# Kernel tuning notes

Hardware: AMD Instinct MI355X
Metric: run time of the kernel (lower is better)

Reference implementation:

```python
import jax, jax.numpy as jnp
import numpy as np

D_MODEL = 1024
N_HEADS = 16
D_K = D_MODEL // N_HEADS


def setup_inputs() -> dict:
    key = jax.random.key(0)
    ks = jax.random.split(key, 16)
    B, S = 2, 2048
    sc = 1.0 / np.sqrt(D_MODEL)
    inp = {
        "query": jax.random.normal(ks[0], (B, S, D_MODEL), jnp.float32),
        "key": jax.random.normal(ks[1], (B, S, D_MODEL), jnp.float32),
        "value": jax.random.normal(ks[2], (B, S, D_MODEL), jnp.float32),
        "Wq": jax.random.normal(ks[3], (D_MODEL, D_MODEL), jnp.float32) * sc,
        "bq": jnp.zeros((D_MODEL,), jnp.float32),
        "Wk": jax.random.normal(ks[4], (D_MODEL, D_MODEL), jnp.float32) * sc,
        "bk": jnp.zeros((D_MODEL,), jnp.float32),
        "Wv": jax.random.normal(ks[5], (D_MODEL, D_MODEL), jnp.float32) * sc,
        "bv": jnp.zeros((D_MODEL,), jnp.float32),
        "Wo": jax.random.normal(ks[6], (D_MODEL, D_MODEL), jnp.float32) * sc,
        "bo": jnp.zeros((D_MODEL,), jnp.float32),
        "theta": jax.random.normal(ks[7], (N_HEADS,), jnp.float32) * 0.1,
        "gate": jax.random.normal(ks[8], (D_MODEL,), jnp.float32) * 0.1,
    }
    return inp


def reference(query, key, value, Wq, bq, Wk, bk, Wv, bv, Wo, bo, theta, gate):
    B, Sq, D = query.shape
    Sk = key.shape[1]
    # linear projections (torch Linear: x @ W.T + b), split heads -> [B,H,S,d_k]
    Q = (query @ Wq.T + bq).reshape(B, Sq, N_HEADS, D_K).transpose(0, 2, 1, 3)
    K = (key @ Wk.T + bk).reshape(B, Sk, N_HEADS, D_K).transpose(0, 2, 1, 3)
    V = (value @ Wv.T + bv).reshape(B, Sk, N_HEADS, D_K).transpose(0, 2, 1, 3)

    inv_sqrt_dk = 1.0 / jnp.sqrt(jnp.float32(D_K))
    scores = jnp.einsum("bhqd,bhkd->bhqk", Q, K) * inv_sqrt_dk

    # per-head rotation of the first two feature dims of Q
    cos_t = jnp.cos(theta)[None, :, None, None]  # [1,H,1,1]
    sin_t = jnp.sin(theta)[None, :, None, None]
    q_rot = jnp.concatenate(
        [
            cos_t * Q[..., :1] - sin_t * Q[..., 1:2],
            sin_t * Q[..., :1] + cos_t * Q[..., 1:2],
            Q[..., 2:],
        ],
        axis=-1,
    )
    scores_q = jnp.einsum("bhqd,bhkd->bhqk", q_rot, K) * inv_sqrt_dk

    g_scalar = jax.nn.sigmoid(gate.mean())
    scores = g_scalar * scores_q + (1.0 - g_scalar) * scores

    attn = jax.nn.softmax(scores, axis=-1)
    out = jnp.einsum("bhqk,bhkd->bhqd", attn, V)
    out = out.transpose(0, 2, 1, 3).reshape(B, Sq, D)
    return out @ Wo.T + bo
```

## Files before the change

### kernel.cpp

```cpp
#include <hip/hip_runtime.h>


typedef __bf16 bf16;
typedef __attribute__((ext_vector_type(8))) bf16 bf16x8;
typedef __attribute__((ext_vector_type(4))) bf16 bf16x4;
typedef __attribute__((ext_vector_type(2))) bf16 bf16x2;
typedef __attribute__((ext_vector_type(4))) float f32x4;
typedef __attribute__((ext_vector_type(4))) short s16x4;
typedef unsigned int u32;

#define D_MODEL 1024
#define NH 16
#define DKH 64
#define SEQ 2048

#define GLL16(g, l) __builtin_amdgcn_global_load_lds(                      \
    (const __attribute__((address_space(1))) void*)(g),                    \
    (__attribute__((address_space(3))) void*)(l), 16, 0, 0)

static __device__ __forceinline__ f32x4 mfma16(bf16x8 a, bf16x8 b, f32x4 c) {
  return __builtin_amdgcn_mfma_f32_16x16x32_bf16(a, b, c, 0, 0, 0);
}

#if __has_builtin(__builtin_amdgcn_mfma_f32_16x16x16bf16_1k)
#define HAVE_MFMA_K16 1
static __device__ __forceinline__ f32x4 mfma16k16(s16x4 a, s16x4 b, f32x4 c) {
  return __builtin_amdgcn_mfma_f32_16x16x16bf16_1k(a, b, c, 0, 0, 0);
}
#else
#define HAVE_MFMA_K16 0
#endif

static __device__ __forceinline__ u32 pk2(float a, float b) {
  bf16x2 v; v[0] = (bf16)a; v[1] = (bf16)b;
  return __builtin_bit_cast(u32, v);
}

static __device__ __forceinline__ float fexp2(float x) {
#if __has_builtin(__builtin_amdgcn_exp2f)
  return __builtin_amdgcn_exp2f(x);
#else
  return exp2f(x);
#endif
}

#define CQK 0.1803368801111244f

__global__ __launch_bounds__(256) void prep(const float* __restrict__ query,
                                            const float* __restrict__ key,
                                            const float* __restrict__ value,
                                            const float* __restrict__ Wq,
                                            const float* __restrict__ bq,
                                            const float* __restrict__ Wk,
                                            const float* __restrict__ Wv,
                                            const float* __restrict__ Wo,
                                            const float* __restrict__ gate,
                                            const float* __restrict__ theta,
                                            bf16* __restrict__ Xq,
                                            bf16* __restrict__ Xk,
                                            bf16* __restrict__ Xv,
                                            bf16* __restrict__ Wqp,
                                            bf16* __restrict__ Wkp,
                                            bf16* __restrict__ Wvp,
                                            bf16* __restrict__ Wop,
                                            float* __restrict__ bqp) {
  const int id = blockIdx.x;
  const int tid = threadIdx.x;
  if (id >= 4096) {
    const int rem = id - 4096;
    const int iz = rem >> 12;
    const int ib = rem & 4095;
    const float* s = (iz == 0) ? query : (iz == 1) ? key : value;
    bf16* d = (iz == 0) ? Xq : (iz == 1) ? Xk : Xv;
    const size_t i = (size_t)(ib * 256 + tid) * 4;
    float4 w = *(const float4*)(s + i);
    bf16x4 o; o[0] = (bf16)w.x; o[1] = (bf16)w.y; o[2] = (bf16)w.z; o[3] = (bf16)w.w;
    *(bf16x4*)(d + i) = o;
    return;
  }
  const int wz = id >> 10, wb = id & 1023;
  if (wz != 0) {
    const float* s = (wz == 1) ? Wk : (wz == 2) ? Wv : Wo;
    bf16* dd = (wz == 1) ? Wkp : (wz == 2) ? Wvp : Wop;
    const size_t i = (size_t)(wb * 256 + tid) * 4;
    float4 v = *(const float4*)(s + i);
    bf16x4 o4; o4[0] = (bf16)v.x; o4[1] = (bf16)v.y; o4[2] = (bf16)v.z; o4[3] = (bf16)v.w;
    *(bf16x4*)(dd + i) = o4;
    return;
  }
  __shared__ float red[4];
  float ssum = 0.f;
  for (int i = tid; i < D_MODEL; i += 256) ssum += gate[i];
#pragma unroll
  for (int off = 32; off > 0; off >>= 1) ssum += __shfl_down(ssum, off);
  if ((tid & 63) == 0) red[tid >> 6] = ssum;
  __syncthreads();
  const float g = 1.f / (1.f + __expf(-(red[0] + red[1] + red[2] + red[3]) / 1024.f));

  const int t = wb * 256 + tid;
  const int r = t >> 8;
  const int c0 = (t & 255) * 4;
  const int d = r & 63, h = r >> 6;
  float4 w = *(const float4*)(Wq + (size_t)r * D_MODEL + c0);
  float4 o;
  if (d == 0) {
    const float a = (g * cosf(theta[h]) + (1.f - g)) * CQK;
    const float bb = (g * sinf(theta[h])) * CQK;
    float4 w2 = *(const float4*)(Wq + (size_t)(r + 1) * D_MODEL + c0);
    o.x = a * w.x - bb * w2.x; o.y = a * w.y - bb * w2.y;
    o.z = a * w.z - bb * w2.z; o.w = a * w.w - bb * w2.w;
    if (c0 == 0) bqp[r] = a * bq[r] - bb * bq[r + 1];
  } else if (d == 1) {
    const float a = (g * cosf(theta[h]) + (1.f - g)) * CQK;
    const float bb = (g * sinf(theta[h])) * CQK;
    float4 w2 = *(const float4*)(Wq + (size_t)(r - 1) * D_MODEL + c0);
    o.x = bb * w2.x + a * w.x; o.y = bb * w2.y + a * w.y;
    o.z = bb * w2.z + a * w.z; o.w = bb * w2.w + a * w.w;
    if (c0 == 0) bqp[r] = bb * bq[r - 1] + a * bq[r];
  } else {
    o.x = CQK * w.x; o.y = CQK * w.y;
    o.z = CQK * w.z; o.w = CQK * w.w;
    if (c0 == 0) bqp[r] = CQK * bq[r];
  }
  bf16x4 ov; ov[0] = (bf16)o.x; ov[1] = (bf16)o.y; ov[2] = (bf16)o.z; ov[3] = (bf16)o.w;
  *(bf16x4*)(Wqp + (size_t)r * D_MODEL + c0) = ov;
}

static __device__ __forceinline__ void gemm_bt_main(const bf16* __restrict__ A,
                                                    const bf16* __restrict__ Bt,
                                                    int tm, int tn, int K,
                                                    f32x4 acc[4][4]) {
  __shared__ bf16 lA[8192];
  __shared__ bf16 lB[8192];
  const int tid = threadIdx.x;
  const int lane = tid & 63, wv = tid >> 6;
  const int wm = wv >> 1, wn = wv & 1;
  const int l16 = lane & 15, lg = lane >> 4;

#pragma unroll
  for (int i = 0; i < 4; ++i)
#pragma unroll
    for (int j = 0; j < 4; ++j) acc[i][j] = (f32x4){0.f, 0.f, 0.f, 0.f};

  int offA[4][2], offB[4][2];
#pragma unroll
  for (int f = 0; f < 4; ++f)
#pragma unroll
    for (int kc = 0; kc < 2; ++kc) {
      const int m = wm * 64 + f * 16 + l16;
      offA[f][kc] = m * 64 + (((kc * 4 + lg) ^ (m & 7)) << 3);
      const int n = wn * 64 + f * 16 + l16;
      offB[f][kc] = n * 64 + (((kc * 4 + lg) ^ (n & 7)) << 3);
    }

  const int rowb = tid >> 3, oct = tid & 7;
  const int soct = oct ^ (rowb & 7);
  const bf16* gA[4];
  const bf16* gB[4];
#pragma unroll
  for (int rd = 0; rd < 4; ++rd) {
    gA[rd] = A + (size_t)(tm + rd * 32 + rowb) * K + soct * 8;
    gB[rd] = Bt + (size_t)(tn + rd * 32 + rowb) * K + soct * 8;
  }

  for (int kt = 0; kt < K; kt += 64) {
    __syncthreads();
#pragma unroll
    for (int rd = 0; rd < 4; ++rd) {
      GLL16(gA[rd] + kt, &lA[rd * 2048 + wv * 512]);
      GLL16(gB[rd] + kt, &lB[rd * 2048 + wv * 512]);
    }
    __syncthreads();
#pragma unroll
    for (int kc = 0; kc < 2; ++kc) {
      bf16x8 af[4], bv[4];
#pragma unroll
      for (int f = 0; f < 4; ++f) {
        af[f] = *(const bf16x8*)&lA[offA[f][kc]];
        bv[f] = *(const bf16x8*)&lB[offB[f][kc]];
      }
#pragma unroll
      for (int i = 0; i < 4; ++i)
#pragma unroll
        for (int j = 0; j < 4; ++j)
          acc[i][j] = mfma16(af[i], bv[j], acc[i][j]);
    }
  }
}

__global__ __launch_bounds__(256) void gemm_qkv(
    const bf16* __restrict__ Xq, const bf16* __restrict__ Xk, const bf16* __restrict__ Xv,
    const bf16* __restrict__ Wq, const bf16* __restrict__ Wk, const bf16* __restrict__ Wv,
    const float* __restrict__ bqp, const float* __restrict__ bk, const float* __restrict__ bv,
    bf16* __restrict__ Qp, bf16* __restrict__ Kp, bf16* __restrict__ Vt) {
  const int wgp = (blockIdx.x & 7) * 96 + (blockIdx.x >> 3);
  const int z = wgp >> 8;
  const int rem = wgp & 255;
  const int tm = (rem >> 3) * 128, tn = (rem & 7) * 128;
  const bf16* A = (z == 0) ? Xq : (z == 1) ? Xk : Xv;
  const bf16* Bt = (z == 0) ? Wq : (z == 1) ? Wk : Wv;
  const float* bias = (z == 0) ? bqp : (z == 1) ? bk : bv;
  f32x4 acc[4][4];
  gemm_bt_main(A, Bt, tm, tn, D_MODEL, acc);
  const int lane = threadIdx.x & 63, wv = threadIdx.x >> 6;
  const int wm = wv >> 1, wn = wv & 1, l16 = lane & 15, lg = lane >> 4;
  if (z < 2) {
    bf16* C = (z == 0) ? Qp : Kp;
#pragma unroll
    for (int i = 0; i < 4; ++i) {
      const int m0 = tm + wm * 64 + i * 16 + lg * 4;
#pragma unroll
      for (int j = 0; j < 4; ++j) {
        const int n = tn + wn * 64 + j * 16 + l16;
        const float bb = bias[n];
        const int h = n >> 6, d = n & 63;
#pragma unroll
        for (int r = 0; r < 4; ++r) {
          const int m = m0 + r;
          const int b = m >> 11, s = m & 2047;
          C[((size_t)(b * NH + h) * SEQ + s) * DKH + d] = (bf16)(acc[i][j][r] + bb);
        }
      }
    }
  } else {
#pragma unroll
    for (int i = 0; i < 4; ++i) {
      const int m0 = tm + wm * 64 + i * 16 + lg * 4;
      const int b = m0 >> 11, s0 = m0 & 2047;
#pragma unroll
      for (int j = 0; j < 4; ++j) {
        const int n = tn + wn * 64 + j * 16 + l16;
        const float bb = bias[n];
        const int h = n >> 6, d = n & 63;
        bf16x4 ov;
#pragma unroll
        for (int r = 0; r < 4; ++r) ov[r] = (bf16)(acc[i][j][r] + bb);
        *(bf16x4*)&Vt[((size_t)(b * NH + h) * DKH + d) * SEQ + s0] = ov;
      }
    }
  }
}

__global__ __launch_bounds__(256) void gemm_out_k(const bf16* __restrict__ A,
                                                  const bf16* __restrict__ Bt,
                                                  const float* __restrict__ bias,
                                                  float* __restrict__ C) {
  const int wgp = (blockIdx.x & 7) * 32 + (blockIdx.x >> 3);
  const int tm = (wgp >> 3) * 128, tn = (wgp & 7) * 128;
  f32x4 acc[4][4];
  gemm_bt_main(A, Bt, tm, tn, D_MODEL, acc);
  const int lane = threadIdx.x & 63, wv = threadIdx.x >> 6;
  const int wm = wv >> 1, wn = wv & 1, l16 = lane & 15, lg = lane >> 4;
#pragma unroll
  for (int i = 0; i < 4; ++i) {
    const int m0 = tm + wm * 64 + i * 16 + lg * 4;
#pragma unroll
    for (int j = 0; j < 4; ++j) {
      const int n = tn + wn * 64 + j * 16 + l16;
      const float bb = bias[n];
#pragma unroll
      for (int r = 0; r < 4; ++r)
        C[(size_t)(m0 + r) * D_MODEL + n] = acc[i][j][r] + bb;
    }
  }
}

__global__ __launch_bounds__(256, 4) void attn_kernel(const bf16* __restrict__ Qp,
                                                      const bf16* __restrict__ Kp,
                                                      const bf16* __restrict__ Vt,
                                                      bf16* __restrict__ Op) {
  __shared__ bf16 lK[4096];
  __shared__ bf16 lV[4096];
#if !HAVE_MFMA_K16
  __shared__ bf16 lP[4096];
#endif

  const int tid = threadIdx.x;
  const int lane = tid & 63, w = tid >> 6;
  const int l16 = lane & 15, lg = lane >> 4;
  const int wgp = (blockIdx.x & 7) * 128 + (blockIdx.x >> 3);
  const int bh = wgp >> 5;
  const int b = bh >> 4, h = bh & 15;
  const int q0 = (wgp & 31) * 64;
  const size_t kvb = (size_t)bh * SEQ * DKH;

  bf16x8 aq[2];
#pragma unroll
  for (int kc = 0; kc < 2; ++kc)
    aq[kc] = *(const bf16x8*)&Qp[kvb + (size_t)(q0 + w * 16 + l16) * DKH + kc * 32 + lg * 8];

  f32x4 o[4];
#pragma unroll
  for (int fn = 0; fn < 4; ++fn) o[fn] = (f32x4){0.f, 0.f, 0.f, 0.f};
  float m_run = -1e30f, l_run = 0.f;

  const int kr = tid >> 3, oct = tid & 7;
  const bf16* gK = Kp + kvb + (size_t)kr * DKH + oct * 8;
  const bf16* gV = Vt + kvb + (size_t)kr * SEQ + oct * 8;
  const int swz0 = kr * 64 + ((oct ^ (kr & 7)) << 3);
  const int swz1 = (kr + 32) * 64 + ((oct ^ (kr & 7)) << 3);

#if !HAVE_MFMA_K16
  bf16* lPw = &lP[w * 1024];
  int pwr[4];
#pragma unroll
  for (int fn = 0; fn < 4; ++fn)
    pwr[fn] = l16 * 64 + (((fn * 2 + (lg >> 1)) ^ (l16 & 7)) << 3) + ((lg & 1) << 2);
  int prd[2];
#pragma unroll
  for (int kc = 0; kc < 2; ++kc)
    prd[kc] = l16 * 64 + (((kc * 4 + lg) ^ (l16 & 7)) << 3);
#endif

  bf16x8 k0r = *(const bf16x8*)(gK);
  bf16x8 k1r = *(const bf16x8*)(gK + 32 * DKH);
  bf16x8 v0r = *(const bf16x8*)(gV);
  bf16x8 v1r = *(const bf16x8*)(gV + (size_t)32 * SEQ);

  for (int kt = 0; kt < SEQ; kt += 64) {
    __syncthreads();
    *(bf16x8*)&lK[swz0] = k0r;  *(bf16x8*)&lK[swz1] = k1r;
    *(bf16x8*)&lV[swz0] = v0r;  *(bf16x8*)&lV[swz1] = v1r;
    __syncthreads();
    if (kt + 64 < SEQ) {
      k0r = *(const bf16x8*)(gK + (size_t)(kt + 64) * DKH);
      k1r = *(const bf16x8*)(gK + (size_t)(kt + 96) * DKH);
      v0r = *(const bf16x8*)(gV + (kt + 64));
      v1r = *(const bf16x8*)(gV + (size_t)32 * SEQ + (kt + 64));
    }

    f32x4 st[4];
    __builtin_amdgcn_s_setprio(1);
#pragma unroll
    for (int fn = 0; fn < 4; ++fn) {
      const int row = fn * 16 + l16;
      bf16x8 ka = *(const bf16x8*)&lK[row * 64 + ((lg ^ (row & 7)) << 3)];
      bf16x8 kb = *(const bf16x8*)&lK[row * 64 + (((4 + lg) ^ (row & 7)) << 3)];
      f32x4 t = (f32x4){0.f, 0.f, 0.f, 0.f};
      t = mfma16(ka, aq[0], t);
      t = mfma16(kb, aq[1], t);
      st[fn] = t;
    }
    __builtin_amdgcn_s_setprio(0);

    float pm = fmaxf(fmaxf(fmaxf(st[0][0], st[0][1]), fmaxf(st[0][2], st[0][3])),
                     fmaxf(fmaxf(st[1][0], st[1][1]), fmaxf(st[1][2], st[1][3])));
    pm = fmaxf(pm, fmaxf(fmaxf(fmaxf(st[2][0], st[2][1]), fmaxf(st[2][2], st[2][3])),
                         fmaxf(fmaxf(st[3][0], st[3][1]), fmaxf(st[3][2], st[3][3]))));
    pm = fmaxf(pm, __shfl_xor(pm, 16));
    pm = fmaxf(pm, __shfl_xor(pm, 32));

    if (!__all(pm <= m_run + 8.f)) {
      const float mnew = fmaxf(m_run, pm);
      const float alpha = fexp2(m_run - mnew);
      m_run = mnew;
      l_run *= alpha;
      float a4[4];
#pragma unroll
      for (int r = 0; r < 4; ++r) a4[r] = __shfl(alpha, (lg << 4) | (lg * 4 + r));
#pragma unroll
      for (int fn = 0; fn < 4; ++fn)
#pragma unroll
        for (int r = 0; r < 4; ++r) o[fn][r] *= a4[r];
    }

    float rs = 0.f;
#if HAVE_MFMA_K16
    s16x4 paf[4];
#endif
#pragma unroll
    for (int fn = 0; fn < 4; ++fn) {
      const float p0 = fexp2(st[fn][0] - m_run);
      const float p1 = fexp2(st[fn][1] - m_run);
      const float p2 = fexp2(st[fn][2] - m_run);
      const float p3 = fexp2(st[fn][3] - m_run);
      rs += (p0 + p1) + (p2 + p3);
      uint2 pw; pw.x = pk2(p0, p1); pw.y = pk2(p2, p3);
#if HAVE_MFMA_K16
      paf[fn] = __builtin_bit_cast(s16x4, pw);
#else
      *(uint2*)&lPw[pwr[fn]] = pw;
#endif
    }
    rs += __shfl_xor(rs, 16);
    rs += __shfl_xor(rs, 32);
    l_run += rs;

    __builtin_amdgcn_s_setprio(1);
#if HAVE_MFMA_K16
#pragma unroll
    for (int dt = 0; dt < 4; ++dt) {
      const int d = dt * 16 + l16;
      const int drow = d * 64, dx = d & 7;
      f32x4 acc = o[dt];
#pragma unroll
      for (int fn = 0; fn < 4; ++fn) {
        const int o2 = (fn * 2 + (lg >> 1)) ^ dx;
        s16x4 vf = *(const s16x4*)&lV[drow + (o2 << 3) + ((lg & 1) << 2)];
        acc = mfma16k16(paf[fn], vf, acc);
      }
      o[dt] = acc;
    }
#else
    bf16x8 pa0 = *(const bf16x8*)&lPw[prd[0]];
    bf16x8 pa1 = *(const bf16x8*)&lPw[prd[1]];
#pragma unroll
    for (int fn = 0; fn < 4; ++fn) {
      const int n = fn * 16 + l16;
      bf16x8 vv0 = *(const bf16x8*)&lV[n * 64 + ((lg ^ (n & 7)) << 3)];
      bf16x8 vv1 = *(const bf16x8*)&lV[n * 64 + (((4 + lg) ^ (n & 7)) << 3)];
      o[fn] = mfma16(pa0, vv0, o[fn]);
      o[fn] = mfma16(pa1, vv1, o[fn]);
    }
#endif
    __builtin_amdgcn_s_setprio(0);
  }

  float linv[4];
#pragma unroll
  for (int r = 0; r < 4; ++r)
    linv[r] = 1.f / __shfl(l_run, (lg << 4) | (lg * 4 + r));
#pragma unroll
  for (int r = 0; r < 4; ++r) {
    const int q = q0 + w * 16 + lg * 4 + r;
#pragma unroll
    for (int fn = 0; fn < 4; ++fn) {
      const int d = fn * 16 + l16;
      Op[((size_t)(b * SEQ + q)) * D_MODEL + h * DKH + d] = (bf16)(o[fn][r] * linv[r]);
    }
  }
}

extern "C" void kernel_launch(void* const* d_in, const int* in_sizes, int n_in,
                              void* d_out, int out_size, void* d_ws, size_t ws_size,
                              hipStream_t stream) {
  (void)in_sizes; (void)n_in; (void)out_size; (void)ws_size;
  const float* query = (const float*)d_in[0];
  const float* key   = (const float*)d_in[1];
  const float* value = (const float*)d_in[2];
  const float* Wq    = (const float*)d_in[3];
  const float* bq    = (const float*)d_in[4];
  const float* Wk    = (const float*)d_in[5];
  const float* bk    = (const float*)d_in[6];
  const float* Wv    = (const float*)d_in[7];
  const float* bv    = (const float*)d_in[8];
  const float* Wo    = (const float*)d_in[9];
  const float* bo    = (const float*)d_in[10];
  const float* theta = (const float*)d_in[11];
  const float* gate  = (const float*)d_in[12];

  float* bqp = (float*)d_ws;
  bf16* wb = (bf16*)((char*)d_ws + 8192);
  bf16* Xq  = wb;
  bf16* Xk  = Xq + 4194304;
  bf16* Xv  = Xk + 4194304;
  bf16* Wqp = Xv + 4194304;
  bf16* Wkp = Wqp + 1048576;
  bf16* Wvp = Wkp + 1048576;
  bf16* Wop = Wvp + 1048576;
  bf16* Qp  = Wop + 1048576;
  bf16* Kp  = Qp + 4194304;
  bf16* Vt  = Kp + 4194304;
  bf16* Op  = Vt + 4194304;

  prep<<<16384, 256, 0, stream>>>(query, key, value, Wq, bq, Wk, Wv, Wo,
                                  gate, theta, Xq, Xk, Xv,
                                  Wqp, Wkp, Wvp, Wop, bqp);
  gemm_qkv<<<768, 256, 0, stream>>>(Xq, Xk, Xv, Wqp, Wkp, Wvp,
                                    bqp, bk, bv, Qp, Kp, Vt);
  attn_kernel<<<1024, 256, 0, stream>>>(Qp, Kp, Vt, Op);
  gemm_out_k<<<256, 256, 0, stream>>>(Op, Wop, bo, (float*)d_out);
}
```

Measured before the change: 142.4 us.

## Double-buffer K/V in LDS and compute row sums via MFMA with ones

Switches the attention loop to double-buffered K/V shared memory tiles with one barrier per iteration, storing the next tile after compute and prefetching two tiles ahead. Replaces the per-lane shuffle-based softmax row-sum with an MFMA against a ones vector that yields the sum already in output layout. Drops the K16 MFMA path so P always round-trips through LDS. This raises LDS use per block (about 40KB), which may limit occupancy, and the row sum is now taken from bf16-rounded probabilities.

```diff
diff --git a/kernel.cpp b/kernel.cpp
--- a/kernel.cpp
+++ b/kernel.cpp
@@ -6,7 +6,6 @@
 typedef __attribute__((ext_vector_type(4))) bf16 bf16x4;
 typedef __attribute__((ext_vector_type(2))) bf16 bf16x2;
 typedef __attribute__((ext_vector_type(4))) float f32x4;
-typedef __attribute__((ext_vector_type(4))) short s16x4;
 typedef unsigned int u32;
 
 #define D_MODEL 1024
@@ -21,15 +20,6 @@
 static __device__ __forceinline__ f32x4 mfma16(bf16x8 a, bf16x8 b, f32x4 c) {
   return __builtin_amdgcn_mfma_f32_16x16x32_bf16(a, b, c, 0, 0, 0);
 }
-
-#if __has_builtin(__builtin_amdgcn_mfma_f32_16x16x16bf16_1k)
-#define HAVE_MFMA_K16 1
-static __device__ __forceinline__ f32x4 mfma16k16(s16x4 a, s16x4 b, f32x4 c) {
-  return __builtin_amdgcn_mfma_f32_16x16x16bf16_1k(a, b, c, 0, 0, 0);
-}
-#else
-#define HAVE_MFMA_K16 0
-#endif
 
 static __device__ __forceinline__ u32 pk2(float a, float b) {
   bf16x2 v; v[0] = (bf16)a; v[1] = (bf16)b;
@@ -269,11 +259,9 @@
                                                       const bf16* __restrict__ Kp,
                                                       const bf16* __restrict__ Vt,
                                                       bf16* __restrict__ Op) {
-  __shared__ bf16 lK[4096];
-  __shared__ bf16 lV[4096];
-#if !HAVE_MFMA_K16
+  __shared__ bf16 lK[2][4096];
+  __shared__ bf16 lV[2][4096];
   __shared__ bf16 lP[4096];
-#endif
 
   const int tid = threadIdx.x;
   const int lane = tid & 63, w = tid >> 6;
@@ -292,7 +280,12 @@
   f32x4 o[4];
 #pragma unroll
   for (int fn = 0; fn < 4; ++fn) o[fn] = (f32x4){0.f, 0.f, 0.f, 0.f};
-  float m_run = -1e30f, l_run = 0.f;
+  f32x4 lacc = (f32x4){0.f, 0.f, 0.f, 0.f};
+  float m_run = -1e30f;
+
+  bf16x8 ones;
+#pragma unroll
+  for (int j = 0; j < 8; ++j) ones[j] = (bf16)1.0f;
 
   const int kr = tid >> 3, oct = tid & 7;
   const bf16* gK = Kp + kvb + (size_t)kr * DKH + oct * 8;
@@ -300,7 +293,6 @@
   const int swz0 = kr * 64 + ((oct ^ (kr & 7)) << 3);
   const int swz1 = (kr + 32) * 64 + ((oct ^ (kr & 7)) << 3);
 
-#if !HAVE_MFMA_K16
   bf16* lPw = &lP[w * 1024];
   int pwr[4];
 #pragma unroll
@@ -310,43 +302,44 @@
 #pragma unroll
   for (int kc = 0; kc < 2; ++kc)
     prd[kc] = l16 * 64 + (((kc * 4 + lg) ^ (l16 & 7)) << 3);
-#endif
 
   bf16x8 k0r = *(const bf16x8*)(gK);
   bf16x8 k1r = *(const bf16x8*)(gK + 32 * DKH);
   bf16x8 v0r = *(const bf16x8*)(gV);
   bf16x8 v1r = *(const bf16x8*)(gV + (size_t)32 * SEQ);
-
-  for (int kt = 0; kt < SEQ; kt += 64) {
-    __syncthreads();
-    *(bf16x8*)&lK[swz0] = k0r;  *(bf16x8*)&lK[swz1] = k1r;
-    *(bf16x8*)&lV[swz0] = v0r;  *(bf16x8*)&lV[swz1] = v1r;
-    __syncthreads();
-    if (kt + 64 < SEQ) {
-      k0r = *(const bf16x8*)(gK + (size_t)(kt + 64) * DKH);
-      k1r = *(const bf16x8*)(gK + (size_t)(kt + 96) * DKH);
-      v0r = *(const bf16x8*)(gV + (kt + 64));
-      v1r = *(const bf16x8*)(gV + (size_t)32 * SEQ + (kt + 64));
-    }
+  *(bf16x8*)&lK[0][swz0] = k0r;  *(bf16x8*)&lK[0][swz1] = k1r;
+  *(bf16x8*)&lV[0][swz0] = v0r;  *(bf16x8*)&lV[0][swz1] = v1r;
+  k0r = *(const bf16x8*)(gK + (size_t)64 * DKH);
+  k1r = *(const bf16x8*)(gK + (size_t)96 * DKH);
+  v0r = *(const bf16x8*)(gV + 64);
+  v1r = *(const bf16x8*)(gV + (size_t)32 * SEQ + 64);
+  __syncthreads();
+
+  for (int t = 0; t < SEQ / 64; ++t) {
+    const bf16* K = &lK[t & 1][0];
+    const bf16* V = &lV[t & 1][0];
 
     f32x4 st[4];
     __builtin_amdgcn_s_setprio(1);
 #pragma unroll
     for (int fn = 0; fn < 4; ++fn) {
       const int row = fn * 16 + l16;
-      bf16x8 ka = *(const bf16x8*)&lK[row * 64 + ((lg ^ (row & 7)) << 3)];
-      bf16x8 kb = *(const bf16x8*)&lK[row * 64 + (((4 + lg) ^ (row & 7)) << 3)];
-      f32x4 t = (f32x4){0.f, 0.f, 0.f, 0.f};
-      t = mfma16(ka, aq[0], t);
-      t = mfma16(kb, aq[1], t);
-      st[fn] = t;
+      bf16x8 ka = *(const bf16x8*)&K[row * 64 + ((lg ^ (row & 7)) << 3)];
+      bf16x8 kb = *(const bf16x8*)&K[row * 64 + (((4 + lg) ^ (row & 7)) << 3)];
+      f32x4 tt = (f32x4){0.f, 0.f, 0.f, 0.f};
+      tt = mfma16(ka, aq[0], tt);
+      tt = mfma16(kb, aq[1], tt);
+      st[fn] = tt;
     }
     __builtin_amdgcn_s_setprio(0);
 
-    float pm = fmaxf(fmaxf(fmaxf(st[0][0], st[0][1]), fmaxf(st[0][2], st[0][3])),
-                     fmaxf(fmaxf(st[1][0], st[1][1]), fmaxf(st[1][2], st[1][3])));
-    pm = fmaxf(pm, fmaxf(fmaxf(fmaxf(st[2][0], st[2][1]), fmaxf(st[2][2], st[2][3])),
-                         fmaxf(fmaxf(st[3][0], st[3][1]), fmaxf(st[3][2], st[3][3]))));
+    const float u0 = fmaxf(fmaxf(st[0][0], st[0][1]), st[0][2]);
+    const float u1 = fmaxf(fmaxf(st[0][3], st[1][0]), st[1][1]);
+    const float u2 = fmaxf(fmaxf(st[1][2], st[1][3]), st[2][0]);
+    const float u3 = fmaxf(fmaxf(st[2][1], st[2][2]), st[2][3]);
+    const float u4 = fmaxf(fmaxf(st[3][0], st[3][1]), st[3][2]);
+    float pm = fmaxf(fmaxf(fmaxf(u0, u1), u2),
+                     fmaxf(fmaxf(u3, u4), st[3][3]));
     pm = fmaxf(pm, __shfl_xor(pm, 16));
     pm = fmaxf(pm, __shfl_xor(pm, 32));
 
@@ -354,72 +347,59 @@
       const float mnew = fmaxf(m_run, pm);
       const float alpha = fexp2(m_run - mnew);
       m_run = mnew;
-      l_run *= alpha;
       float a4[4];
 #pragma unroll
       for (int r = 0; r < 4; ++r) a4[r] = __shfl(alpha, (lg << 4) | (lg * 4 + r));
 #pragma unroll
+      for (int r = 0; r < 4; ++r) lacc[r] *= a4[r];
+#pragma unroll
       for (int fn = 0; fn < 4; ++fn)
 #pragma unroll
         for (int r = 0; r < 4; ++r) o[fn][r] *= a4[r];
     }
 
-    float rs = 0.f;
-#if HAVE_MFMA_K16
-    s16x4 paf[4];
-#endif
 #pragma unroll
     for (int fn = 0; fn < 4; ++fn) {
-      const float p0 = fexp2(st[fn][0] - m_run);
-      const float p1 = fexp2(st[fn][1] - m_run);
-      const float p2 = fexp2(st[fn][2] - m_run);
-      const float p3 = fexp2(st[fn][3] - m_run);
-      rs += (p0 + p1) + (p2 + p3);
-      uint2 pw; pw.x = pk2(p0, p1); pw.y = pk2(p2, p3);
-#if HAVE_MFMA_K16
-      paf[fn] = __builtin_bit_cast(s16x4, pw);
-#else
+      uint2 pw;
+      pw.x = pk2(fexp2(st[fn][0] - m_run), fexp2(st[fn][1] - m_run));
+      pw.y = pk2(fexp2(st[fn][2] - m_run), fexp2(st[fn][3] - m_run));
       *(uint2*)&lPw[pwr[fn]] = pw;
-#endif
-    }
-    rs += __shfl_xor(rs, 16);
-    rs += __shfl_xor(rs, 32);
-    l_run += rs;
-
-    __builtin_amdgcn_s_setprio(1);
-#if HAVE_MFMA_K16
-#pragma unroll
-    for (int dt = 0; dt < 4; ++dt) {
-      const int d = dt * 16 + l16;
-      const int drow = d * 64, dx = d & 7;
-      f32x4 acc = o[dt];
-#pragma unroll
-      for (int fn = 0; fn < 4; ++fn) {
-        const int o2 = (fn * 2 + (lg >> 1)) ^ dx;
-        s16x4 vf = *(const s16x4*)&lV[drow + (o2 << 3) + ((lg & 1) << 2)];
-        acc = mfma16k16(paf[fn], vf, acc);
-      }
-      o[dt] = acc;
-    }
-#else
+    }
+
     bf16x8 pa0 = *(const bf16x8*)&lPw[prd[0]];
     bf16x8 pa1 = *(const bf16x8*)&lPw[prd[1]];
+
+    __builtin_amdgcn_s_setprio(1);
+    lacc = mfma16(pa0, ones, lacc);
+    lacc = mfma16(pa1, ones, lacc);
 #pragma unroll
     for (int fn = 0; fn < 4; ++fn) {
       const int n = fn * 16 + l16;
-      bf16x8 vv0 = *(const bf16x8*)&lV[n * 64 + ((lg ^ (n & 7)) << 3)];
-      bf16x8 vv1 = *(const bf16x8*)&lV[n * 64 + (((4 + lg) ^ (n & 7)) << 3)];
+      bf16x8 vv0 = *(const bf16x8*)&V[n * 64 + ((lg ^ (n & 7)) << 3)];
+      bf16x8 vv1 = *(const bf16x8*)&V[n * 64 + (((4 + lg) ^ (n & 7)) << 3)];
       o[fn] = mfma16(pa0, vv0, o[fn]);
       o[fn] = mfma16(pa1, vv1, o[fn]);
     }
-#endif
     __builtin_amdgcn_s_setprio(0);
+
+    if (t + 1 < SEQ / 64) {
+      const int nb = (t + 1) & 1;
+      *(bf16x8*)&lK[nb][swz0] = k0r;  *(bf16x8*)&lK[nb][swz1] = k1r;
+      *(bf16x8*)&lV[nb][swz0] = v0r;  *(bf16x8*)&lV[nb][swz1] = v1r;
+      if (t + 2 < SEQ / 64) {
+        const int kt2 = (t + 2) * 64;
+        k0r = *(const bf16x8*)(gK + (size_t)kt2 * DKH);
+        k1r = *(const bf16x8*)(gK + (size_t)(kt2 + 32) * DKH);
+        v0r = *(const bf16x8*)(gV + kt2);
+        v1r = *(const bf16x8*)(gV + (size_t)32 * SEQ + kt2);
+      }
+    }
+    __syncthreads();
   }
 
   float linv[4];
 #pragma unroll
-  for (int r = 0; r < 4; ++r)
-    linv[r] = 1.f / __shfl(l_run, (lg << 4) | (lg * 4 + r));
+  for (int r = 0; r < 4; ++r) linv[r] = 1.f / lacc[r];
 #pragma unroll
   for (int r = 0; r < 4; ++r) {
     const int q = q0 + w * 16 + lg * 4 + r;
```

New measurement: 134.8 us. 1.06x faster.
